# Kernel optimization log

Hardware: AMD Instinct MI355X
Metric: run time of the kernel (lower is better)

Reference implementation:

```python
import jax, jax.numpy as jnp
import numpy as np

B, L, D, NH, DH = 2, 1024, 1024, 16, 2048
HD, HDH = D // NH, DH // NH


def _linear(x, w, b):
    return x @ w.T + b


def _silu(x):
    return x * jax.nn.sigmoid(x)


def _silu_backward(x):
    s = jax.nn.sigmoid(x)
    sil = x * s
    return sil + s * (1.0 - sil)


def setup_inputs() -> dict:
    key = jax.random.key(0)
    ks = jax.random.split(key, 20)
    scale = 0.02
    x = jax.random.normal(ks[0], (B, L, D), dtype=jnp.float32)
    W1 = jax.random.normal(ks[1], (B, NH, HDH, HD), dtype=jnp.float32) * scale
    W2 = jax.random.normal(ks[2], (B, NH, HD, HDH), dtype=jnp.float32) * scale
    log_base_lr = jnp.ones((NH,), jnp.float32) * np.float32(np.log(0.01))
    log_base_weight_decay = jnp.ones((NH,), jnp.float32) * np.float32(np.log(0.1))
    fc_lr_w = jax.random.normal(ks[3], (NH, D), jnp.float32) * scale
    fc_lr_b = jnp.zeros((NH,), jnp.float32)
    fc_wd_w = jax.random.normal(ks[4], (NH, D), jnp.float32) * scale
    fc_wd_b = jnp.zeros((NH,), jnp.float32)
    q_w = jax.random.normal(ks[5], (D, D), jnp.float32) * scale
    q_b = jnp.zeros((D,), jnp.float32)
    k_w = jax.random.normal(ks[6], (D, D), jnp.float32) * scale
    k_b = jnp.zeros((D,), jnp.float32)
    v_w = jax.random.normal(ks[7], (D, D), jnp.float32) * scale
    v_b = jnp.zeros((D,), jnp.float32)
    o_w = jax.random.normal(ks[8], (D, D), jnp.float32) * scale
    o_b = jnp.zeros((D,), jnp.float32)
    return {"x": x, "W1": W1, "W2": W2,
            "log_base_lr": log_base_lr, "fc_lr_w": fc_lr_w, "fc_lr_b": fc_lr_b,
            "log_base_weight_decay": log_base_weight_decay, "fc_wd_w": fc_wd_w, "fc_wd_b": fc_wd_b,
            "q_w": q_w, "q_b": q_b, "k_w": k_w, "k_b": k_b,
            "v_w": v_w, "v_b": v_b, "o_w": o_w, "o_b": o_b}


def reference(x, W1, W2, log_base_lr, fc_lr_w, fc_lr_b, log_base_weight_decay,
              fc_wd_w, fc_wd_b, q_w, q_b, k_w, k_b, v_w, v_b, o_w, o_b):
    batch, length, dim = x.shape
    nh = W1.shape[1]
    hd = dim // nh
    # projections -> [b, n, l, d]
    query = _linear(x, q_w, q_b).reshape(batch, length, nh, hd).transpose(0, 2, 1, 3)
    key = _linear(x, k_w, k_b).reshape(batch, length, nh, hd).transpose(0, 2, 1, 3)
    value = _linear(x, v_w, v_b).reshape(batch, length, nh, hd).transpose(0, 2, 1, 3)
    # per-token, per-head learning rate and weight decay  [b, n, l]
    lr = jnp.exp(log_base_lr)[None, :, None] * jax.nn.sigmoid(_linear(x, fc_lr_w, fc_lr_b)).transpose(0, 2, 1)
    log_wd = jnp.log1p(-jnp.exp(log_base_weight_decay)[None, :, None]
                       * jax.nn.sigmoid(_linear(x, fc_wd_w, fc_wd_b)).transpose(0, 2, 1))
    wd_cross = jnp.exp(jnp.cumsum(log_wd, axis=2))  # [b, n, l]
    # [b, n, m, l] decay mask: exp(sum_{j=m+1}^{l} log_wd_j) on upper triangle
    lw_rep = jnp.broadcast_to(log_wd[:, :, None, :], (batch, nh, length, length))
    wd_inner = jnp.triu(jnp.exp(jnp.cumsum(jnp.triu(lw_rep, 1), axis=3)))
    # two-layer MLP memory forward on keys
    X1 = key
    Z1 = jnp.einsum('bnhd,bnld->bnlh', W1, X1)
    X2 = _silu(Z1)
    Z2 = jnp.einsum('bndh,bnlh->bnld', W2, X2)
    grad_Z2 = Z2 - value
    grad_X2 = jnp.einsum('bndh,bnld->bnlh', W2, grad_Z2)
    grad_Z1 = _silu_backward(Z1) * grad_X2
    # layer-1 readout at queries with chunked delta-rule correction
    X1_ = query
    mask_X1X1_ = jnp.einsum('bnld,bnmd->bnlm', X1, X1_) * wd_inner
    Z1_ = (-jnp.einsum('bnlh,bnl,bnlm->bnmh', grad_Z1, lr, mask_X1X1_)
           + jnp.einsum('bnhd,bnld,bnl->bnlh', W1, X1_, wd_cross))
    W1_next = (-jnp.einsum('bnlh,bnl,bnld->bnhd', grad_Z1, lr * wd_inner[:, :, :, -1], X1)
               + W1 * wd_cross[:, :, -1][:, :, None, None])
    # layer-2 readout
    X2_ = _silu(Z1_)
    mask_X2X2_ = jnp.einsum('bnlh,bnmh->bnlm', X2, X2_) * wd_inner
    Z2_ = (-jnp.einsum('bnld,bnl,bnlm->bnmd', grad_Z2, lr, mask_X2X2_)
           + jnp.einsum('bndh,bnlh,bnl->bnld', W2, X2_, wd_cross))
    W2_next = (-jnp.einsum('bnld,bnl,bnlh->bndh', grad_Z2, lr * wd_inner[:, :, :, -1], X2)
               + W2 * wd_cross[:, :, -1][:, :, None, None])
    out = _linear(Z2_.transpose(0, 2, 1, 3).reshape(batch, length, dim), o_w, o_b)
    return out, W1_next, W2_next
```

## Files before the change

kernel.cpp:

```cpp
#include <hip/hip_runtime.h>

constexpr int CB = 2, CL = 1024, CD = 1024, CNH = 16, CHD = 64, CHDH = 128, CBN = CB * CNH;

__device__ __forceinline__ float sigf(float x) { return 1.0f / (1.0f + __expf(-x)); }

__device__ __forceinline__ unsigned short f2bf(float x) {
    unsigned u = __float_as_uint(x);
    u += 0x7fffu + ((u >> 16) & 1u);
    return (unsigned short)(u >> 16);
}
__device__ __forceinline__ unsigned pk2(float a, float b) {
    return (unsigned)f2bf(a) | ((unsigned)f2bf(b) << 16);
}
__device__ __forceinline__ unsigned pkus(unsigned short a, unsigned short b) {
    return (unsigned)a | ((unsigned)b << 16);
}
__device__ __forceinline__ float bf2f(unsigned short u) {
    return __uint_as_float(((unsigned)u) << 16);
}

typedef __attribute__((ext_vector_type(8))) short short8v;
typedef __attribute__((ext_vector_type(4))) float f32x4;
#define MFMA16(a, b, c) __builtin_amdgcn_mfma_f32_16x16x32_bf16(a, b, c, 0, 0, 0)

__global__ __launch_bounds__(256) void conv_kernel(
    const float* __restrict__ x, const float* __restrict__ qw,
    const float* __restrict__ kw, const float* __restrict__ vw,
    const float* __restrict__ W1, const float* __restrict__ W2,
    const float* __restrict__ ow, unsigned short* __restrict__ xb,
    unsigned short* __restrict__ qwb, unsigned short* __restrict__ kwb,
    unsigned short* __restrict__ vwb, unsigned short* __restrict__ w1b,
    unsigned short* __restrict__ w2b, unsigned short* __restrict__ w2t,
    unsigned short* __restrict__ owh, unsigned short* __restrict__ owl) {
    int i = blockIdx.x * 256 + threadIdx.x;
    if (i < 1310720) {
        const float* s;
        unsigned short* d;
        int off;
        if (i < 524288) { s = x; d = xb; off = i; }
        else if (i < 786432) { s = qw; d = qwb; off = i - 524288; }
        else if (i < 1048576) { s = kw; d = kwb; off = i - 786432; }
        else { s = vw; d = vwb; off = i - 1048576; }
        float4 v = *(const float4*)(s + (size_t)off * 4);
        *(uint2*)(d + (size_t)off * 4) = make_uint2(pk2(v.x, v.y), pk2(v.z, v.w));
    } else if (i < 1507328) {
        int j = i - 1310720;
        if (j < 65536) {
            size_t e = (size_t)j * 4;
            float4 v = *(const float4*)(W1 + e);
            *(uint2*)(w1b + e) = make_uint2(pk2(v.x, v.y), pk2(v.z, v.w));
        } else if (j < 131072) {
            size_t e = (size_t)(j - 65536) * 4;
            float4 v = *(const float4*)(W2 + e);
            *(uint2*)(w2b + e) = make_uint2(pk2(v.x, v.y), pk2(v.z, v.w));
        } else {
            size_t e = (size_t)(j - 131072) * 4;
            int bn = (int)(e >> 13), rem = (int)(e & 8191);
            int h = rem >> 6, d0 = rem & 63;
            const float* src = W2 + (size_t)bn * CHD * CHDH;
            float a = src[(d0 + 0) * CHDH + h], b = src[(d0 + 1) * CHDH + h];
            float c = src[(d0 + 2) * CHDH + h], dd = src[(d0 + 3) * CHDH + h];
            *(uint2*)(w2t + e) = make_uint2(pk2(a, b), pk2(c, dd));
        }
    } else {
        size_t e = (size_t)(i - 1507328) * 4;
        float4 v = *(const float4*)(ow + e);
        unsigned short h0 = f2bf(v.x), h1 = f2bf(v.y), h2 = f2bf(v.z), h3 = f2bf(v.w);
        *(uint2*)(owh + e) = make_uint2(pkus(h0, h1), pkus(h2, h3));
        *(uint2*)(owl + e) = make_uint2(
            pk2(v.x - bf2f(h0), v.y - bf2f(h1)), pk2(v.z - bf2f(h2), v.w - bf2f(h3)));
    }
}

__global__ __launch_bounds__(512) void qkv_mfma(
    const unsigned short* __restrict__ xbf, const unsigned short* __restrict__ wqkv,
    const float* __restrict__ qb, const float* __restrict__ kb,
    const float* __restrict__ vb, unsigned short* __restrict__ qbf,
    unsigned short* __restrict__ kbf, unsigned short* __restrict__ ktbf,
    float* __restrict__ vhb) {
    __shared__ __align__(16) unsigned short SM[26112];
    unsigned short(*Ab)[136] = (unsigned short(*)[136])SM;
    unsigned short(*Bb)[136] = (unsigned short(*)[136])(SM + 8704);
    const int t = threadIdx.x;
    const int c0 = blockIdx.x << 7, r0 = blockIdx.y << 6;
    const int wv = t >> 6, lane = t & 63;
    const int lm = lane & 15, lg = lane >> 4;
    f32x4 acc[4];
#pragma unroll
    for (int i = 0; i < 4; ++i) acc[i] = (f32x4){0.f, 0.f, 0.f, 0.f};
    for (int kc = 0; kc < CD; kc += 128) {
        for (int i = t; i < 1024; i += 512) {
            int r = i >> 4, c = (i & 15) * 8;
            *(uint4*)&Ab[r][c] = *(const uint4*)(xbf + (size_t)(r0 + r) * CD + kc + c);
        }
        for (int i = t; i < 2048; i += 512) {
            int r = i >> 4, c = (i & 15) * 8;
            *(uint4*)&Bb[r][c] = *(const uint4*)(wqkv + (size_t)(c0 + r) * CD + kc + c);
        }
        __syncthreads();
#pragma unroll
        for (int m16 = 0; m16 < 4; ++m16)
#pragma unroll
            for (int ks = 0; ks < 4; ++ks) {
                short8v a = *(const short8v*)&Ab[m16 * 16 + lm][ks * 32 + lg * 8];
                short8v b = *(const short8v*)&Bb[wv * 16 + lm][ks * 32 + lg * 8];
                acc[m16] = MFMA16(a, b, acc[m16]);
            }
        __syncthreads();
    }
    const int which = c0 >> 10;
    const int ccb = c0 & 1023;
    const float* bias = which == 0 ? qb : (which == 1 ? kb : vb);
    const int b = r0 >> 10, lb0 = r0 & 1023;
    float(*Os)[132] = (float(*)[132])SM;
    {
        int col = wv * 16 + lm;
        float bb = bias[ccb + col];
#pragma unroll
        for (int m16 = 0; m16 < 4; ++m16)
#pragma unroll
            for (int r = 0; r < 4; ++r)
                Os[m16 * 16 + lg * 4 + r][col] = acc[m16][r] + bb;
    }
    __syncthreads();
    if (which == 2) {
        for (int i = t; i < 2048; i += 512) {
            int r = i >> 5, c = (i & 31) * 4;
            int n = (ccb + c) >> 6, d = (ccb + c) & 63;
            *(float4*)(vhb + (((size_t)b * CNH + n) * CL + lb0 + r) * 64 + d) =
                *(const float4*)&Os[r][c];
        }
    } else {
        unsigned short* dst = which == 0 ? qbf : kbf;
        for (int i = t; i < 2048; i += 512) {
            int r = i >> 5, c = (i & 31) * 4;
            int n = (ccb + c) >> 6, d = (ccb + c) & 63;
            float4 v4 = *(const float4*)&Os[r][c];
            *(uint2*)(dst + (((size_t)b * CNH + n) * CL + lb0 + r) * 64 + d) =
                make_uint2(pk2(v4.x, v4.y), pk2(v4.z, v4.w));
        }
        if (which == 1) {
            for (int i = t; i < 1024; i += 512) {
                int col = i >> 3, lb = (i & 7) * 8;
                int n = (ccb + col) >> 6, d = (ccb + col) & 63;
                uint4 u;
                u.x = pk2(Os[lb + 0][col], Os[lb + 1][col]);
                u.y = pk2(Os[lb + 2][col], Os[lb + 3][col]);
                u.z = pk2(Os[lb + 4][col], Os[lb + 5][col]);
                u.w = pk2(Os[lb + 6][col], Os[lb + 7][col]);
                *(uint4*)(ktbf + (((size_t)b * CNH + n) * 64 + d) * CL + lb0 + lb) = u;
            }
        }
    }
}

__global__ __launch_bounds__(512) void gemm_obf(const unsigned short* __restrict__ zh,
                                                const unsigned short* __restrict__ zl,
                                                const unsigned short* __restrict__ Bh,
                                                const unsigned short* __restrict__ Bl,
                                                const float* __restrict__ bias,
                                                float* __restrict__ C) {
    __shared__ __align__(16) unsigned short SM[52224];
    unsigned short(*Ah)[136] = (unsigned short(*)[136])SM;
    unsigned short(*Al)[136] = (unsigned short(*)[136])(SM + 8704);
    unsigned short(*Bhs)[136] = (unsigned short(*)[136])(SM + 17408);
    unsigned short(*Bls)[136] = (unsigned short(*)[136])(SM + 34816);
    const int t = threadIdx.x;
    const int r0 = blockIdx.x << 6, c0 = blockIdx.y << 7;
    const int wv = t >> 6, lane = t & 63;
    const int lm = lane & 15, lg = lane >> 4;
    const int b = r0 >> 10, lb0 = r0 & 1023;
    f32x4 acc[4];
#pragma unroll
    for (int i = 0; i < 4; ++i) acc[i] = (f32x4){0.f, 0.f, 0.f, 0.f};
    for (int kc = 0; kc < CD; kc += 128) {
        for (int i = t; i < 1024; i += 512) {
            int r = i >> 4, c = (i & 15) * 8;
            int k = kc + c, n = k >> 6, d = k & 63;
            size_t abase = (((size_t)b * CNH + n) * CL + lb0 + r) * 64 + d;
            *(uint4*)&Ah[r][c] = *(const uint4*)(zh + abase);
            *(uint4*)&Al[r][c] = *(const uint4*)(zl + abase);
        }
        for (int i = t; i < 2048; i += 512) {
            int r = i >> 4, c = (i & 15) * 8;
            *(uint4*)&Bhs[r][c] = *(const uint4*)(Bh + (size_t)(c0 + r) * CD + kc + c);
            *(uint4*)&Bls[r][c] = *(const uint4*)(Bl + (size_t)(c0 + r) * CD + kc + c);
        }
        __syncthreads();
#pragma unroll
        for (int m16 = 0; m16 < 4; ++m16)
#pragma unroll
            for (int ks = 0; ks < 4; ++ks) {
                short8v ah = *(const short8v*)&Ah[m16 * 16 + lm][ks * 32 + lg * 8];
                short8v al = *(const short8v*)&Al[m16 * 16 + lm][ks * 32 + lg * 8];
                short8v bh = *(const short8v*)&Bhs[wv * 16 + lm][ks * 32 + lg * 8];
                short8v bl = *(const short8v*)&Bls[wv * 16 + lm][ks * 32 + lg * 8];
                acc[m16] = MFMA16(ah, bh, acc[m16]);
                acc[m16] = MFMA16(ah, bl, acc[m16]);
                acc[m16] = MFMA16(al, bh, acc[m16]);
            }
        __syncthreads();
    }
    float(*Os)[132] = (float(*)[132])SM;
    {
        int col = wv * 16 + lm;
        float bb = bias[c0 + col];
#pragma unroll
        for (int m16 = 0; m16 < 4; ++m16)
#pragma unroll
            for (int r = 0; r < 4; ++r)
                Os[m16 * 16 + lg * 4 + r][col] = acc[m16][r] + bb;
    }
    __syncthreads();
    for (int i = t; i < 2048; i += 512) {
        int r = i >> 5, c = (i & 31) * 4;
        *(float4*)(C + (size_t)(r0 + r) * CD + c0 + c) = *(const float4*)&Os[r][c];
    }
}

__global__ __launch_bounds__(256) void lrwd_kernel(
    const float* __restrict__ x, const float* __restrict__ lblr,
    const float* __restrict__ fclr_w, const float* __restrict__ fclr_b,
    const float* __restrict__ lbwd, const float* __restrict__ fcwd_w,
    const float* __restrict__ fcwd_b, float* __restrict__ lrp,
    float* __restrict__ logwd) {
    const int r = blockIdx.x;
    const int b = r >> 10, l = r & 1023;
    const int wv = threadIdx.x >> 6, lane = threadIdx.x & 63;
    float xv[16];
#pragma unroll
    for (int j = 0; j < 16; ++j) xv[j] = x[(size_t)r * CD + lane + 64 * j];
    for (int j = 0; j < 4; ++j) {
        const int n = wv * 4 + j;
        float d1 = 0.f, d2 = 0.f;
#pragma unroll
        for (int k = 0; k < 16; ++k) {
            d1 += xv[k] * fclr_w[(size_t)n * CD + lane + 64 * k];
            d2 += xv[k] * fcwd_w[(size_t)n * CD + lane + 64 * k];
        }
#pragma unroll
        for (int s = 32; s > 0; s >>= 1) {
            d1 += __shfl_down(d1, s);
            d2 += __shfl_down(d2, s);
        }
        if (lane == 0) {
            lrp[((size_t)b * CNH + n) * CL + l] = __expf(lblr[n]) * sigf(d1 + fclr_b[n]);
            logwd[((size_t)b * CNH + n) * CL + l] =
                log1pf(-__expf(lbwd[n]) * sigf(d2 + fcwd_b[n]));
        }
    }
}

__global__ __launch_bounds__(64) void scan_kernel(float* __restrict__ cum,
                                                  float* __restrict__ wdc) {
    const int bn = blockIdx.x;
    const int lane = threadIdx.x;
    float* p = cum + (size_t)bn * CL;
    float v[16];
#pragma unroll
    for (int j = 0; j < 16; ++j) v[j] = p[lane * 16 + j];
#pragma unroll
    for (int j = 1; j < 16; ++j) v[j] += v[j - 1];
    float tot = v[15];
    float inc = tot;
#pragma unroll
    for (int s = 1; s < 64; s <<= 1) {
        float tv = __shfl_up(inc, s);
        if (lane >= s) inc += tv;
    }
    const float pre = inc - tot;
#pragma unroll
    for (int j = 0; j < 16; ++j) {
        float c = pre + v[j];
        p[lane * 16 + j] = c;
        wdc[(size_t)bn * CL + lane * 16 + j] = __expf(c);
    }
}

__global__ __launch_bounds__(256) void mlp_mfma(
    const unsigned short* __restrict__ kbf, const float* __restrict__ vh,
    const unsigned short* __restrict__ w1bf, const unsigned short* __restrict__ w2bf,
    const unsigned short* __restrict__ w2tbf, unsigned short* __restrict__ x2bf,
    unsigned short* __restrict__ x2t, unsigned short* __restrict__ gz1t,
    unsigned short* __restrict__ gz2t) {
    __shared__ __align__(16) unsigned short RA[128][72];
    __shared__ __align__(16) unsigned short RB[64][72];
    __shared__ __align__(16) unsigned short RC[64][136];
    __shared__ __align__(16) unsigned short X2s[64][136];
    const int bn = blockIdx.y, l0 = blockIdx.x << 6;
    const int t = threadIdx.x;
    const int wv = t >> 6, lane = t & 63;
    const int lm = lane & 15, lg = lane >> 4;
    {
        const unsigned short* kg = kbf + ((size_t)bn * CL + l0) * CHD;
        for (int i = t; i < 512; i += 256) {
            int r = i >> 3, c = (i & 7) * 8;
            *(uint4*)&RB[r][c] = *(const uint4*)(kg + (size_t)r * CHD + c);
        }
        const unsigned short* w1g = w1bf + (size_t)bn * CHDH * CHD;
        for (int i = t; i < 1024; i += 256) {
            int r = i >> 3, c = (i & 7) * 8;
            *(uint4*)&RA[r][c] = *(const uint4*)(w1g + (size_t)r * CHD + c);
        }
        const unsigned short* w2g = w2bf + (size_t)bn * CHD * CHDH;
        for (int i = t; i < 1024; i += 256) {
            int r = i >> 4, c = (i & 15) * 8;
            *(uint4*)&RC[r][c] = *(const uint4*)(w2g + (size_t)r * CHDH + c);
        }
    }
    __syncthreads();
    f32x4 acc1[4][2];
#pragma unroll
    for (int i = 0; i < 4; ++i)
#pragma unroll
        for (int j = 0; j < 2; ++j) acc1[i][j] = (f32x4){0.f, 0.f, 0.f, 0.f};
#pragma unroll
    for (int m16 = 0; m16 < 4; ++m16)
#pragma unroll
        for (int hh = 0; hh < 2; ++hh) {
            int h16 = wv * 2 + hh;
#pragma unroll
            for (int ks = 0; ks < 2; ++ks) {
                short8v a = *(const short8v*)&RB[m16 * 16 + lm][ks * 32 + lg * 8];
                short8v b = *(const short8v*)&RA[h16 * 16 + lm][ks * 32 + lg * 8];
                acc1[m16][hh] = MFMA16(a, b, acc1[m16][hh]);
            }
        }
#pragma unroll
    for (int m16 = 0; m16 < 4; ++m16)
#pragma unroll
        for (int hh = 0; hh < 2; ++hh)
#pragma unroll
            for (int r = 0; r < 4; ++r) {
                float a = acc1[m16][hh][r];
                X2s[m16 * 16 + lg * 4 + r][(wv * 2 + hh) * 16 + lm] = f2bf(a * sigf(a));
            }
    __syncthreads();
    {
        const unsigned short* w2tg = w2tbf + (size_t)bn * CHDH * CHD;
        for (int i = t; i < 1024; i += 256) {
            int r = i >> 3, c = (i & 7) * 8;
            *(uint4*)&RA[r][c] = *(const uint4*)(w2tg + (size_t)r * CHD + c);
        }
    }
    {
        f32x4 acc2[4];
#pragma unroll
        for (int i = 0; i < 4; ++i) acc2[i] = (f32x4){0.f, 0.f, 0.f, 0.f};
#pragma unroll
        for (int m16 = 0; m16 < 4; ++m16)
#pragma unroll
            for (int ks = 0; ks < 4; ++ks) {
                short8v a = *(const short8v*)&X2s[m16 * 16 + lm][ks * 32 + lg * 8];
                short8v b = *(const short8v*)&RC[wv * 16 + lm][ks * 32 + lg * 8];
                acc2[m16] = MFMA16(a, b, acc2[m16]);
            }
#pragma unroll
        for (int m16 = 0; m16 < 4; ++m16)
#pragma unroll
            for (int r = 0; r < 4; ++r) {
                int l = l0 + m16 * 16 + lg * 4 + r;
                float v = vh[((size_t)bn * CL + l) * 64 + wv * 16 + lm];
                RB[m16 * 16 + lg * 4 + r][wv * 16 + lm] = f2bf(acc2[m16][r] - v);
            }
    }
    __syncthreads();
#pragma unroll
    for (int m16 = 0; m16 < 4; ++m16)
#pragma unroll
        for (int hh = 0; hh < 2; ++hh) {
            int h16 = wv * 2 + hh;
            f32x4 p = (f32x4){0.f, 0.f, 0.f, 0.f};
#pragma unroll
            for (int ks = 0; ks < 2; ++ks) {
                short8v a = *(const short8v*)&RB[m16 * 16 + lm][ks * 32 + lg * 8];
                short8v b = *(const short8v*)&RA[h16 * 16 + lm][ks * 32 + lg * 8];
                p = MFMA16(a, b, p);
            }
#pragma unroll
            for (int r = 0; r < 4; ++r) {
                float zz = acc1[m16][hh][r];
                float s = sigf(zz);
                float sil = zz * s;
                RC[m16 * 16 + lg * 4 + r][h16 * 16 + lm] =
                    f2bf((sil + s * (1.f - sil)) * p[r]);
            }
        }
    __syncthreads();
    for (int i = t; i < 1024; i += 256) {
        int r = i >> 4, c = (i & 15) * 8;
        *(uint4*)(x2bf + ((size_t)bn * CL + l0 + r) * CHDH + c) = *(const uint4*)&X2s[r][c];
    }
    for (int i = t; i < 1024; i += 256) {
        int h = i >> 3, lb = (i & 7) * 8;
        uint4 u;
        u.x = pkus(X2s[lb + 0][h], X2s[lb + 1][h]);
        u.y = pkus(X2s[lb + 2][h], X2s[lb + 3][h]);
        u.z = pkus(X2s[lb + 4][h], X2s[lb + 5][h]);
        u.w = pkus(X2s[lb + 6][h], X2s[lb + 7][h]);
        *(uint4*)(x2t + ((size_t)bn * CHDH + h) * CL + l0 + lb) = u;
    }
    for (int i = t; i < 1024; i += 256) {
        int h = i >> 3, lb = (i & 7) * 8;
        uint4 u;
        u.x = pkus(RC[lb + 0][h], RC[lb + 1][h]);
        u.y = pkus(RC[lb + 2][h], RC[lb + 3][h]);
        u.z = pkus(RC[lb + 4][h], RC[lb + 5][h]);
        u.w = pkus(RC[lb + 6][h], RC[lb + 7][h]);
        *(uint4*)(gz1t + ((size_t)bn * CHDH + h) * CL + l0 + lb) = u;
    }
    for (int i = t; i < 512; i += 256) {
        int d = i >> 3, lb = (i & 7) * 8;
        uint4 u;
        u.x = pkus(RB[lb + 0][d], RB[lb + 1][d]);
        u.y = pkus(RB[lb + 2][d], RB[lb + 3][d]);
        u.z = pkus(RB[lb + 4][d], RB[lb + 5][d]);
        u.w = pkus(RB[lb + 6][d], RB[lb + 7][d]);
        *(uint4*)(gz2t + ((size_t)bn * CHD + d) * CL + l0 + lb) = u;
    }
}

__global__ __launch_bounds__(256) void dsA1(
    const unsigned short* __restrict__ ktbf, const unsigned short* __restrict__ gz1t,
    const float* __restrict__ lrp, const float* __restrict__ cump,
    float* __restrict__ ds1, float* __restrict__ ds2) {
    __shared__ __align__(16) unsigned short Ab[64][72];
    __shared__ __align__(16) unsigned short Bb[128][72];
    __shared__ float coefA[64];
    const int c = blockIdx.x, bn = blockIdx.y, t = threadIdx.x;
    const int l0 = c << 6;
    const int wv = t >> 6, lane = t & 63;
    const int lm = lane & 15, lg = lane >> 4;
    const float Ac = cump[(size_t)bn * CL + l0];
    if (t < 64)
        coefA[t] = lrp[(size_t)bn * CL + l0 + t] *
                   __expf(Ac - cump[(size_t)bn * CL + l0 + t]);
    for (int i = t; i < 1024; i += 256) {
        int h = i >> 3, cc = (i & 7) * 8;
        *(uint4*)&Bb[h][cc] = *(const uint4*)(gz1t + ((size_t)bn * CHDH + h) * CL + l0 + cc);
    }
    __syncthreads();
    for (int i = t; i < 512; i += 256) {
        int d = i >> 3, cc = (i & 7) * 8;
        uint4 g = *(const uint4*)(ktbf + ((size_t)bn * CHD + d) * CL + l0 + cc);
        unsigned short* gp = (unsigned short*)&g;
        uint4 o;
        o.x = pk2(bf2f(gp[0]) * coefA[cc + 0], bf2f(gp[1]) * coefA[cc + 1]);
        o.y = pk2(bf2f(gp[2]) * coefA[cc + 2], bf2f(gp[3]) * coefA[cc + 3]);
        o.z = pk2(bf2f(gp[4]) * coefA[cc + 4], bf2f(gp[5]) * coefA[cc + 5]);
        o.w = pk2(bf2f(gp[6]) * coefA[cc + 6], bf2f(gp[7]) * coefA[cc + 7]);
        *(uint4*)&Ab[d][cc] = o;
    }
    __syncthreads();
    f32x4 acc[8];
#pragma unroll
    for (int i = 0; i < 8; ++i) acc[i] = (f32x4){0.f, 0.f, 0.f, 0.f};
#pragma unroll
    for (int h16 = 0; h16 < 8; ++h16)
#pragma unroll
        for (int ks = 0; ks < 2; ++ks) {
            short8v a = *(const short8v*)&Ab[wv * 16 + lm][ks * 32 + lg * 8];
            short8v b = *(const short8v*)&Bb[h16 * 16 + lm][ks * 32 + lg * 8];
            acc[h16] = MFMA16(a, b, acc[h16]);
        }
    float* og = (bn < 16 ? ds1 : ds2) + ((size_t)(((bn & 15) << 4) + c) << 13);
#pragma unroll
    for (int h16 = 0; h16 < 8; ++h16)
#pragma unroll
        for (int r = 0; r < 4; ++r)
            og[(wv * 16 + lg * 4 + r) * 128 + h16 * 16 + lm] = acc[h16][r];
}

__global__ __launch_bounds__(256) void dsB1(
    const float* __restrict__ ds1, const float* __restrict__ ds2,
    const float* __restrict__ cump, const float* __restrict__ W1,
    unsigned short* __restrict__ sp1, float* __restrict__ w1n) {
    __shared__ float anch[16];
    const int g = blockIdx.x, bn = blockIdx.y, t = threadIdx.x;
    if (t < 16) anch[t] = cump[(size_t)bn * CL + (t << 6)];
    __syncthreads();
    const float ccl = cump[(size_t)bn * CL + CL - 1];
    const float wdcl = __expf(ccl);
    const float* dS = (bn < 16 ? ds1 : ds2) + ((size_t)((bn & 15) << 4) << 13);
    unsigned short* spb = sp1 + ((size_t)bn << 17);
    const int e0 = g << 10;
    float s[4];
#pragma unroll
    for (int j = 0; j < 4; ++j) s[j] = 0.f;
    for (int c = 0; c < 16; ++c) {
        if (c > 0) {
            float fac = __expf(anch[c] - anch[c - 1]);
            const float* dp = dS + ((size_t)(c - 1) << 13);
#pragma unroll
            for (int j = 0; j < 4; ++j) s[j] = fac * (s[j] + dp[e0 + j * 256 + t]);
        }
        unsigned short* so = spb + ((size_t)c << 13);
#pragma unroll
        for (int j = 0; j < 4; ++j) so[e0 + j * 256 + t] = f2bf(s[j]);
    }
    const float ex = __expf(ccl - anch[15]);
    const float* dp = dS + ((size_t)15 << 13);
    const float* w1g = W1 + ((size_t)bn << 13);
    float* og = w1n + ((size_t)bn << 13);
#pragma unroll
    for (int j = 0; j < 4; ++j) {
        int e = e0 + j * 256 + t;
        int d = e >> 7, h = e & 127;
        float full = s[j] + dp[e];
        og[h * 64 + d] = wdcl * w1g[h * 64 + d] - ex * full;
    }
}

__global__ __launch_bounds__(256) void dsC1(
    const unsigned short* __restrict__ qbf, const unsigned short* __restrict__ kbf,
    const unsigned short* __restrict__ gz1t, const unsigned short* __restrict__ w1bf,
    const unsigned short* __restrict__ sp1, const float* __restrict__ lrp,
    const float* __restrict__ cump, const float* __restrict__ wdcp,
    unsigned short* __restrict__ x2q) {
    __shared__ __align__(16) unsigned short Qb[64][72];
    __shared__ __align__(16) unsigned short XB[128][72];
    __shared__ __align__(16) unsigned short Kb[64][72];
    __shared__ __align__(16) unsigned short GT[128][72];
    __shared__ __align__(16) unsigned short Pm[64][72];
    __shared__ float lrc[64], cumc[64], wdcc[64];
    const int c = blockIdx.x, bn = blockIdx.y, t = threadIdx.x;
    const int l0 = c << 6;
    const int w4 = t >> 6, lane = t & 63;
    const int lm = lane & 15, lg = lane >> 4;
    {
        const unsigned short* qg = qbf + ((size_t)bn * CL + l0) * CHD;
        for (int i = t; i < 512; i += 256) {
            int r = i >> 3, cc = (i & 7) * 8;
            *(uint4*)&Qb[r][cc] = *(const uint4*)(qg + (size_t)r * CHD + cc);
        }
        const unsigned short* wg = w1bf + (size_t)bn * CHDH * CHD;
        for (int i = t; i < 1024; i += 256) {
            int r = i >> 3, cc = (i & 7) * 8;
            *(uint4*)&XB[r][cc] = *(const uint4*)(wg + (size_t)r * CHD + cc);
        }
        if (t < 64) {
            lrc[t] = lrp[(size_t)bn * CL + l0 + t];
            cumc[t] = cump[(size_t)bn * CL + l0 + t];
            wdcc[t] = wdcp[(size_t)bn * CL + l0 + t];
        }
    }
    __syncthreads();
    const float Ac = cumc[0];
    short8v qf[4][2];
#pragma unroll
    for (int m16 = 0; m16 < 4; ++m16)
#pragma unroll
        for (int ks = 0; ks < 2; ++ks)
            qf[m16][ks] = *(const short8v*)&Qb[m16 * 16 + lm][ks * 32 + lg * 8];
    f32x4 acc[4][2];
#pragma unroll
    for (int i = 0; i < 4; ++i)
#pragma unroll
        for (int j = 0; j < 2; ++j) acc[i][j] = (f32x4){0.f, 0.f, 0.f, 0.f};
    {
        short8v wf[2][2];
#pragma unroll
        for (int hh = 0; hh < 2; ++hh)
#pragma unroll
            for (int ks = 0; ks < 2; ++ks)
                wf[hh][ks] =
                    *(const short8v*)&XB[(w4 * 2 + hh) * 16 + lm][ks * 32 + lg * 8];
#pragma unroll
        for (int m16 = 0; m16 < 4; ++m16)
#pragma unroll
            for (int hh = 0; hh < 2; ++hh)
#pragma unroll
                for (int ks = 0; ks < 2; ++ks)
                    acc[m16][hh] = MFMA16(qf[m16][ks], wf[hh][ks], acc[m16][hh]);
#pragma unroll
        for (int m16 = 0; m16 < 4; ++m16)
#pragma unroll
            for (int r = 0; r < 4; ++r) {
                float w = wdcc[m16 * 16 + lg * 4 + r];
                acc[m16][0][r] *= w;
                acc[m16][1][r] *= w;
            }
    }
    __syncthreads();
    {
        const unsigned short* sb = sp1 + ((((size_t)bn << 4) + c) << 13);
        for (int i = t; i < 1024; i += 256) {
            int d = i >> 4, hg = (i & 15) * 8;
            uint4 u = *(const uint4*)(sb + d * 128 + hg);
            const unsigned short* up = (const unsigned short*)&u;
#pragma unroll
            for (int j = 0; j < 8; ++j) XB[hg + j][d] = up[j];
        }
    }
    __syncthreads();
    {
        short8v sf[2][2];
#pragma unroll
        for (int hh = 0; hh < 2; ++hh)
#pragma unroll
            for (int ks = 0; ks < 2; ++ks)
                sf[hh][ks] =
                    *(const short8v*)&XB[(w4 * 2 + hh) * 16 + lm][ks * 32 + lg * 8];
#pragma unroll
        for (int m16 = 0; m16 < 4; ++m16)
#pragma unroll
            for (int hh = 0; hh < 2; ++hh) {
                f32x4 pf = (f32x4){0.f, 0.f, 0.f, 0.f};
#pragma unroll
                for (int ks = 0; ks < 2; ++ks)
                    pf = MFMA16(qf[m16][ks], sf[hh][ks], pf);
#pragma unroll
                for (int r = 0; r < 4; ++r) {
                    float em = __expf(cumc[m16 * 16 + lg * 4 + r] - Ac);
                    acc[m16][hh][r] -= em * pf[r];
                }
            }
    }
    __syncthreads();
    {
        const unsigned short* kg = kbf + ((size_t)bn * CL + l0) * CHD;
        for (int i = t; i < 512; i += 256) {
            int r = i >> 3, cc = (i & 7) * 8;
            *(uint4*)&Kb[r][cc] = *(const uint4*)(kg + (size_t)r * CHD + cc);
        }
        const unsigned short* gg = gz1t + (size_t)bn * CHDH * CL + l0;
        for (int i = t; i < 1024; i += 256) {
            int r = i >> 3, cc = (i & 7) * 8;
            *(uint4*)&GT[r][cc] = *(const uint4*)(gg + (size_t)r * CL + cc);
        }
    }
    __syncthreads();
    {
        short8v kf[2];
#pragma unroll
        for (int ks = 0; ks < 2; ++ks)
            kf[ks] = *(const short8v*)&Kb[w4 * 16 + lm][ks * 32 + lg * 8];
#pragma unroll
        for (int m16 = 0; m16 < 4; ++m16) {
            f32x4 s = (f32x4){0.f, 0.f, 0.f, 0.f};
#pragma unroll
            for (int ks = 0; ks < 2; ++ks) s = MFMA16(kf[ks], qf[m16][ks], s);
            int mloc = m16 * 16 + lm;
            float cm = cumc[mloc];
            unsigned short pv[4];
#pragma unroll
            for (int r = 0; r < 4; ++r) {
                int lloc = w4 * 16 + lg * 4 + r;
                float val = (mloc >= lloc)
                                ? s[r] * lrc[lloc] * __expf(cm - cumc[lloc])
                                : 0.f;
                pv[r] = f2bf(val);
            }
            *(uint2*)&Pm[mloc][w4 * 16 + lg * 4] =
                make_uint2(pkus(pv[0], pv[1]), pkus(pv[2], pv[3]));
        }
    }
    __syncthreads();
    {
        short8v gt[2][2], pm[4][2];
#pragma unroll
        for (int hh = 0; hh < 2; ++hh)
#pragma unroll
            for (int ks = 0; ks < 2; ++ks)
                gt[hh][ks] =
                    *(const short8v*)&GT[(w4 * 2 + hh) * 16 + lm][ks * 32 + lg * 8];
#pragma unroll
        for (int m16 = 0; m16 < 4; ++m16)
#pragma unroll
            for (int ks = 0; ks < 2; ++ks)
                pm[m16][ks] = *(const short8v*)&Pm[m16 * 16 + lm][ks * 32 + lg * 8];
#pragma unroll
        for (int m16 = 0; m16 < 4; ++m16)
#pragma unroll
            for (int hh = 0; hh < 2; ++hh) {
                f32x4 pf = (f32x4){0.f, 0.f, 0.f, 0.f};
#pragma unroll
                for (int ks = 0; ks < 2; ++ks) pf = MFMA16(pm[m16][ks], gt[hh][ks], pf);
#pragma unroll
                for (int r = 0; r < 4; ++r) acc[m16][hh][r] -= pf[r];
            }
    }
    __syncthreads();
    {
        unsigned short(*Ob)[136] = (unsigned short(*)[136])XB;
#pragma unroll
        for (int m16 = 0; m16 < 4; ++m16)
#pragma unroll
            for (int hh = 0; hh < 2; ++hh) {
                int h = (w4 * 2 + hh) * 16 + lm;
#pragma unroll
                for (int r = 0; r < 4; ++r) {
                    float a = acc[m16][hh][r];
                    Ob[m16 * 16 + lg * 4 + r][h] = f2bf(a * sigf(a));
                }
            }
        __syncthreads();
        unsigned short* og = x2q + ((size_t)bn * CL + l0) * CHDH;
        for (int i = t; i < 1024; i += 256) {
            int r = i >> 4, cc = (i & 15) * 8;
            *(uint4*)(og + (size_t)r * CHDH + cc) = *(const uint4*)&Ob[r][cc];
        }
    }
}

__global__ __launch_bounds__(256) void dsA2(
    const unsigned short* __restrict__ x2t, const unsigned short* __restrict__ gz2t,
    const float* __restrict__ lrp, const float* __restrict__ cump,
    float* __restrict__ ds1, float* __restrict__ ds2) {
    __shared__ __align__(16) unsigned short Ab[128][72];
    __shared__ __align__(16) unsigned short Bb[64][72];
    __shared__ float coefA[64];
    const int c = blockIdx.x, bn = blockIdx.y, t = threadIdx.x;
    const int l0 = c << 6;
    const int wv = t >> 6, lane = t & 63;
    const int lm = lane & 15, lg = lane >> 4;
    const float Ac = cump[(size_t)bn * CL + l0];
    if (t < 64)
        coefA[t] = lrp[(size_t)bn * CL + l0 + t] *
                   __expf(Ac - cump[(size_t)bn * CL + l0 + t]);
    for (int i = t; i < 512; i += 256) {
        int d = i >> 3, cc = (i & 7) * 8;
        *(uint4*)&Bb[d][cc] = *(const uint4*)(gz2t + ((size_t)bn * CHD + d) * CL + l0 + cc);
    }
    __syncthreads();
    for (int i = t; i < 1024; i += 256) {
        int h = i >> 3, cc = (i & 7) * 8;
        uint4 g = *(const uint4*)(x2t + ((size_t)bn * CHDH + h) * CL + l0 + cc);
        unsigned short* gp = (unsigned short*)&g;
        uint4 o;
        o.x = pk2(bf2f(gp[0]) * coefA[cc + 0], bf2f(gp[1]) * coefA[cc + 1]);
        o.y = pk2(bf2f(gp[2]) * coefA[cc + 2], bf2f(gp[3]) * coefA[cc + 3]);
        o.z = pk2(bf2f(gp[4]) * coefA[cc + 4], bf2f(gp[5]) * coefA[cc + 5]);
        o.w = pk2(bf2f(gp[6]) * coefA[cc + 6], bf2f(gp[7]) * coefA[cc + 7]);
        *(uint4*)&Ab[h][cc] = o;
    }
    __syncthreads();
    f32x4 acc[2][4];
#pragma unroll
    for (int i = 0; i < 2; ++i)
#pragma unroll
        for (int j = 0; j < 4; ++j) acc[i][j] = (f32x4){0.f, 0.f, 0.f, 0.f};
#pragma unroll
    for (int mm = 0; mm < 2; ++mm) {
        int hk16 = wv * 2 + mm;
#pragma unroll
        for (int d16 = 0; d16 < 4; ++d16)
#pragma unroll
            for (int ks = 0; ks < 2; ++ks) {
                short8v a = *(const short8v*)&Ab[hk16 * 16 + lm][ks * 32 + lg * 8];
                short8v b = *(const short8v*)&Bb[d16 * 16 + lm][ks * 32 + lg * 8];
                acc[mm][d16] = MFMA16(a, b, acc[mm][d16]);
            }
    }
    float* og = (bn < 16 ? ds1 : ds2) + ((size_t)(((bn & 15) << 4) + c) << 13);
#pragma unroll
    for (int mm = 0; mm < 2; ++mm)
#pragma unroll
        for (int d16 = 0; d16 < 4; ++d16)
#pragma unroll
            for (int r = 0; r < 4; ++r)
                og[((wv * 2 + mm) * 16 + lg * 4 + r) * 64 + d16 * 16 + lm] =
                    acc[mm][d16][r];
}

__global__ __launch_bounds__(256) void dsB2(
    const float* __restrict__ ds1, const float* __restrict__ ds2,
    const float* __restrict__ cump, const float* __restrict__ W2,
    unsigned short* __restrict__ sp2, float* __restrict__ w2n) {
    __shared__ float anch[16];
    const int g = blockIdx.x, bn = blockIdx.y, t = threadIdx.x;
    if (t < 16) anch[t] = cump[(size_t)bn * CL + (t << 6)];
    __syncthreads();
    const float ccl = cump[(size_t)bn * CL + CL - 1];
    const float wdcl = __expf(ccl);
    const float* dS = (bn < 16 ? ds1 : ds2) + ((size_t)((bn & 15) << 4) << 13);
    unsigned short* spb = sp2 + ((size_t)bn << 17);
    const int e0 = g << 10;
    float s[4];
#pragma unroll
    for (int j = 0; j < 4; ++j) s[j] = 0.f;
    for (int c = 0; c < 16; ++c) {
        if (c > 0) {
            float fac = __expf(anch[c] - anch[c - 1]);
            const float* dp = dS + ((size_t)(c - 1) << 13);
#pragma unroll
            for (int j = 0; j < 4; ++j) s[j] = fac * (s[j] + dp[e0 + j * 256 + t]);
        }
        unsigned short* so = spb + ((size_t)c << 13);
#pragma unroll
        for (int j = 0; j < 4; ++j) so[e0 + j * 256 + t] = f2bf(s[j]);
    }
    const float ex = __expf(ccl - anch[15]);
    const float* dp = dS + ((size_t)15 << 13);
    const float* w2g = W2 + ((size_t)bn << 13);
    float* og = w2n + ((size_t)bn << 13);
#pragma unroll
    for (int j = 0; j < 4; ++j) {
        int e = e0 + j * 256 + t;
        int hk = e >> 6, d = e & 63;
        float full = s[j] + dp[e];
        og[d * 128 + hk] = wdcl * w2g[d * 128 + hk] - ex * full;
    }
}

__global__ __launch_bounds__(256) void dsC2(
    const unsigned short* __restrict__ x2q, const unsigned short* __restrict__ x2bf,
    const unsigned short* __restrict__ gz2t, const unsigned short* __restrict__ w2bf,
    const unsigned short* __restrict__ sp2, const float* __restrict__ lrp,
    const float* __restrict__ cump, const float* __restrict__ wdcp,
    unsigned short* __restrict__ zh, unsigned short* __restrict__ zl) {
    __shared__ __align__(16) unsigned short X2qb[64][136];
    __shared__ __align__(16) unsigned short XB[64][136];
    __shared__ __align__(16) unsigned short GT2[64][72];
    __shared__ __align__(16) unsigned short Pm[64][72];
    __shared__ float lrc[64], cumc[64], wdcc[64];
    const int c = blockIdx.x, bn = blockIdx.y, t = threadIdx.x;
    const int l0 = c << 6;
    const int w4 = t >> 6, lane = t & 63;
    const int lm = lane & 15, lg = lane >> 4;
    {
        const unsigned short* qg = x2q + ((size_t)bn * CL + l0) * CHDH;
        for (int i = t; i < 1024; i += 256) {
            int r = i >> 4, cc = (i & 15) * 8;
            *(uint4*)&X2qb[r][cc] = *(const uint4*)(qg + (size_t)r * CHDH + cc);
        }
        const unsigned short* wg = w2bf + (size_t)bn * CHD * CHDH;
        for (int i = t; i < 1024; i += 256) {
            int r = i >> 4, cc = (i & 15) * 8;
            *(uint4*)&XB[r][cc] = *(const uint4*)(wg + (size_t)r * CHDH + cc);
        }
        if (t < 64) {
            lrc[t] = lrp[(size_t)bn * CL + l0 + t];
            cumc[t] = cump[(size_t)bn * CL + l0 + t];
            wdcc[t] = wdcp[(size_t)bn * CL + l0 + t];
        }
    }
    __syncthreads();
    const float Ac = cumc[0];
    short8v qf[4][4];
#pragma unroll
    for (int m16 = 0; m16 < 4; ++m16)
#pragma unroll
        for (int ks = 0; ks < 4; ++ks)
            qf[m16][ks] = *(const short8v*)&X2qb[m16 * 16 + lm][ks * 32 + lg * 8];
    f32x4 acc[4];
#pragma unroll
    for (int i = 0; i < 4; ++i) acc[i] = (f32x4){0.f, 0.f, 0.f, 0.f};
    {
        short8v wf[4];
#pragma unroll
        for (int ks = 0; ks < 4; ++ks)
            wf[ks] = *(const short8v*)&XB[w4 * 16 + lm][ks * 32 + lg * 8];
#pragma unroll
        for (int m16 = 0; m16 < 4; ++m16)
#pragma unroll
            for (int ks = 0; ks < 4; ++ks)
                acc[m16] = MFMA16(qf[m16][ks], wf[ks], acc[m16]);
#pragma unroll
        for (int m16 = 0; m16 < 4; ++m16)
#pragma unroll
            for (int r = 0; r < 4; ++r)
                acc[m16][r] *= wdcc[m16 * 16 + lg * 4 + r];
    }
    __syncthreads();
    {
        const unsigned short* sb = sp2 + ((((size_t)bn << 4) + c) << 13);
        for (int i = t; i < 1024; i += 256) {
            int hk = i >> 3, dg = (i & 7) * 8;
            uint4 u = *(const uint4*)(sb + hk * 64 + dg);
            const unsigned short* up = (const unsigned short*)&u;
#pragma unroll
            for (int j = 0; j < 8; ++j) XB[dg + j][hk] = up[j];
        }
    }
    __syncthreads();
    {
        short8v sf[4];
#pragma unroll
        for (int ks = 0; ks < 4; ++ks)
            sf[ks] = *(const short8v*)&XB[w4 * 16 + lm][ks * 32 + lg * 8];
#pragma unroll
        for (int m16 = 0; m16 < 4; ++m16) {
            f32x4 pf = (f32x4){0.f, 0.f, 0.f, 0.f};
#pragma unroll
            for (int ks = 0; ks < 4; ++ks) pf = MFMA16(qf[m16][ks], sf[ks], pf);
#pragma unroll
            for (int r = 0; r < 4; ++r) {
                float em = __expf(cumc[m16 * 16 + lg * 4 + r] - Ac);
                acc[m16][r] -= em * pf[r];
            }
        }
    }
    __syncthreads();
    {
        const unsigned short* kg = x2bf + ((size_t)bn * CL + l0) * CHDH;
        for (int i = t; i < 1024; i += 256) {
            int r = i >> 4, cc = (i & 15) * 8;
            *(uint4*)&XB[r][cc] = *(const uint4*)(kg + (size_t)r * CHDH + cc);
        }
        const unsigned short* gg = gz2t + (size_t)bn * CHD * CL + l0;
        for (int i = t; i < 512; i += 256) {
            int r = i >> 3, cc = (i & 7) * 8;
            *(uint4*)&GT2[r][cc] = *(const uint4*)(gg + (size_t)r * CL + cc);
        }
    }
    __syncthreads();
    {
        short8v kf[4];
#pragma unroll
        for (int ks = 0; ks < 4; ++ks)
            kf[ks] = *(const short8v*)&XB[w4 * 16 + lm][ks * 32 + lg * 8];
#pragma unroll
        for (int m16 = 0; m16 < 4; ++m16) {
            f32x4 s = (f32x4){0.f, 0.f, 0.f, 0.f};
#pragma unroll
            for (int ks = 0; ks < 4; ++ks) s = MFMA16(kf[ks], qf[m16][ks], s);
            int mloc = m16 * 16 + lm;
            float cm = cumc[mloc];
            unsigned short pv[4];
#pragma unroll
            for (int r = 0; r < 4; ++r) {
                int lloc = w4 * 16 + lg * 4 + r;
                float val = (mloc >= lloc)
                                ? s[r] * lrc[lloc] * __expf(cm - cumc[lloc])
                                : 0.f;
                pv[r] = f2bf(val);
            }
            *(uint2*)&Pm[mloc][w4 * 16 + lg * 4] =
                make_uint2(pkus(pv[0], pv[1]), pkus(pv[2], pv[3]));
        }
    }
    __syncthreads();
    {
        short8v gt[2], pm[4][2];
#pragma unroll
        for (int ks = 0; ks < 2; ++ks)
            gt[ks] = *(const short8v*)&GT2[w4 * 16 + lm][ks * 32 + lg * 8];
#pragma unroll
        for (int m16 = 0; m16 < 4; ++m16)
#pragma unroll
            for (int ks = 0; ks < 2; ++ks)
                pm[m16][ks] = *(const short8v*)&Pm[m16 * 16 + lm][ks * 32 + lg * 8];
#pragma unroll
        for (int m16 = 0; m16 < 4; ++m16) {
            f32x4 pf = (f32x4){0.f, 0.f, 0.f, 0.f};
#pragma unroll
            for (int ks = 0; ks < 2; ++ks) pf = MFMA16(pm[m16][ks], gt[ks], pf);
#pragma unroll
            for (int r = 0; r < 4; ++r) acc[m16][r] -= pf[r];
        }
    }
    __syncthreads();
    {
        float(*Os)[68] = (float(*)[68])X2qb;
#pragma unroll
        for (int m16 = 0; m16 < 4; ++m16)
#pragma unroll
            for (int r = 0; r < 4; ++r)
                Os[m16 * 16 + lg * 4 + r][w4 * 16 + lm] = acc[m16][r];
        __syncthreads();
        unsigned short* zhg = zh + ((size_t)bn * CL + l0) * CHD;
        unsigned short* zlg = zl + ((size_t)bn * CL + l0) * CHD;
        for (int i = t; i < 1024; i += 256) {
            int r = i >> 4, cc = (i & 15) << 2;
            float4 v = *(const float4*)&Os[r][cc];
            unsigned short h0 = f2bf(v.x), h1 = f2bf(v.y), h2 = f2bf(v.z), h3 = f2bf(v.w);
            *(uint2*)(zhg + (size_t)r * CHD + cc) = make_uint2(pkus(h0, h1), pkus(h2, h3));
            *(uint2*)(zlg + (size_t)r * CHD + cc) = make_uint2(
                pk2(v.x - bf2f(h0), v.y - bf2f(h1)), pk2(v.z - bf2f(h2), v.w - bf2f(h3)));
        }
    }
}

extern "C" void kernel_launch(void* const* d_in, const int* in_sizes, int n_in,
                              void* d_out, int out_size, void* d_ws, size_t ws_size,
                              hipStream_t stream) {
    (void)in_sizes; (void)n_in; (void)out_size; (void)ws_size;
    const float* x      = (const float*)d_in[0];
    const float* W1     = (const float*)d_in[1];
    const float* W2     = (const float*)d_in[2];
    const float* lblr   = (const float*)d_in[3];
    const float* fclr_w = (const float*)d_in[4];
    const float* fclr_b = (const float*)d_in[5];
    const float* lbwd   = (const float*)d_in[6];
    const float* fcwd_w = (const float*)d_in[7];
    const float* fcwd_b = (const float*)d_in[8];
    const float* qw = (const float*)d_in[9];
    const float* qb = (const float*)d_in[10];
    const float* kw = (const float*)d_in[11];
    const float* kb = (const float*)d_in[12];
    const float* vw = (const float*)d_in[13];
    const float* vb = (const float*)d_in[14];
    const float* ow = (const float*)d_in[15];
    const float* ob = (const float*)d_in[16];

    float* ws = (float*)d_ws;
    const size_t SZ_HD = (size_t)CBN * CL * CHD;
    const size_t SZ_HDH = (size_t)CBN * CL * CHDH;
    float* qh   = ws;
    float* khb  = qh + SZ_HD;
    float* vhb  = khb + SZ_HD;
    float* gz2b = vhb + SZ_HD;
    float* z2sb = gz2b + SZ_HD;
    float* x2b  = z2sb + SZ_HD;
    float* gz1b = x2b + SZ_HDH;
    float* x2qb = gz1b + SZ_HDH;
    float* lrb  = x2qb + SZ_HDH;
    float* cumb = lrb + (size_t)CBN * CL;
    float* wdcb = cumb + (size_t)CBN * CL;
    unsigned short* xbf  = (unsigned short*)(wdcb + (size_t)CBN * CL);
    unsigned short* qwbf = xbf + (size_t)CB * CL * CD;
    unsigned short* kwbf = qwbf + (size_t)CD * CD;
    unsigned short* vwbf = kwbf + (size_t)CD * CD;
    unsigned short* owh  = vwbf + (size_t)CD * CD;
    unsigned short* owl  = owh + (size_t)CD * CD;

    unsigned short* qbf   = (unsigned short*)qh;
    unsigned short* kbf   = qbf + SZ_HD;
    unsigned short* ktbf  = (unsigned short*)khb;
    unsigned short* w1bf  = ktbf + SZ_HD;
    unsigned short* w2bf  = w1bf + (size_t)CBN * CHDH * CHD;
    unsigned short* w2tbf = w2bf + (size_t)CBN * CHDH * CHD;
    unsigned short* gz2t  = (unsigned short*)gz2b;
    unsigned short* x2t   = (unsigned short*)x2b;
    unsigned short* gz1t  = (unsigned short*)gz1b;
    unsigned short* x2q   = (unsigned short*)x2qb;
    unsigned short* x2bf  = x2q + SZ_HDH;
    float* ds1 = gz1b + 2097152;
    float* ds2 = x2b + 2097152;
    unsigned short* sp1 = (unsigned short*)vhb;
    unsigned short* sp2 = (unsigned short*)vhb;
    unsigned short* zh = (unsigned short*)z2sb;
    unsigned short* zl = zh + SZ_HD;

    float* outp = (float*)d_out;
    float* w1n = outp + (size_t)CB * CL * CD;
    float* w2n = w1n + (size_t)CBN * CHDH * CHD;

    conv_kernel<<<6912, 256, 0, stream>>>(x, qw, kw, vw, W1, W2, ow, xbf, qwbf, kwbf,
                                          vwbf, w1bf, w2bf, w2tbf, owh, owl);
    qkv_mfma<<<dim3(24, 32), 512, 0, stream>>>(xbf, qwbf, qb, kb, vb, qbf, kbf, ktbf,
                                               vhb);
    lrwd_kernel<<<CB * CL, 256, 0, stream>>>(x, lblr, fclr_w, fclr_b, lbwd, fcwd_w,
                                             fcwd_b, lrb, cumb);
    scan_kernel<<<CBN, 64, 0, stream>>>(cumb, wdcb);
    mlp_mfma<<<dim3(CL / 64, CBN), 256, 0, stream>>>(kbf, vhb, w1bf, w2bf, w2tbf,
                                                     x2bf, x2t, gz1t, gz2t);
    dsA1<<<dim3(16, CBN), 256, 0, stream>>>(ktbf, gz1t, lrb, cumb, ds1, ds2);
    dsB1<<<dim3(8, CBN), 256, 0, stream>>>(ds1, ds2, cumb, W1, sp1, w1n);
    dsC1<<<dim3(16, CBN), 256, 0, stream>>>(qbf, kbf, gz1t, w1bf, sp1, lrb, cumb,
                                            wdcb, x2q);
    dsA2<<<dim3(16, CBN), 256, 0, stream>>>(x2t, gz2t, lrb, cumb, ds1, ds2);
    dsB2<<<dim3(8, CBN), 256, 0, stream>>>(ds1, ds2, cumb, W2, sp2, w2n);
    dsC2<<<dim3(16, CBN), 256, 0, stream>>>(x2q, x2bf, gz2t, w2bf, sp2, lrb, cumb,
                                            wdcb, zh, zl);
    gemm_obf<<<dim3(32, 8), 512, 0, stream>>>(zh, zl, owh, owl, ob, outp);
}
```

Measured before the change: 168.6 us.

## Prefetch all chunk operands into dedicated LDS buffers and drop intermediate barriers

In the two chunked readout kernels (dsC1 and dsC2), the single reused LDS staging buffer is split into separate buffers for W, the chunk state, keys and the transposed gradient. All of these are loaded at kernel start instead of in staged phases, which removes several __syncthreads barriers and lets the global loads overlap with each other. The cost is much more LDS per block, which can cut how many blocks fit on a CU. The removal of some barriers before aliased output staging also depends on later barriers for correctness.

Result: slower. 180.6 us (+7.1%).

```diff
diff --git a/kernel.cpp b/kernel.cpp
--- a/kernel.cpp
+++ b/kernel.cpp
@@ -518,7 +518,8 @@
     const float* __restrict__ cump, const float* __restrict__ wdcp,
     unsigned short* __restrict__ x2q) {
     __shared__ __align__(16) unsigned short Qb[64][72];
-    __shared__ __align__(16) unsigned short XB[128][72];
+    __shared__ __align__(16) unsigned short W1b[128][72];
+    __shared__ __align__(16) unsigned short S1[128][72];
     __shared__ __align__(16) unsigned short Kb[64][72];
     __shared__ __align__(16) unsigned short GT[128][72];
     __shared__ __align__(16) unsigned short Pm[64][72];
@@ -536,7 +537,25 @@
         const unsigned short* wg = w1bf + (size_t)bn * CHDH * CHD;
         for (int i = t; i < 1024; i += 256) {
             int r = i >> 3, cc = (i & 7) * 8;
-            *(uint4*)&XB[r][cc] = *(const uint4*)(wg + (size_t)r * CHD + cc);
+            *(uint4*)&W1b[r][cc] = *(const uint4*)(wg + (size_t)r * CHD + cc);
+        }
+        const unsigned short* sb = sp1 + ((((size_t)bn << 4) + c) << 13);
+        for (int i = t; i < 1024; i += 256) {
+            int d = i >> 4, hg = (i & 15) * 8;
+            uint4 u = *(const uint4*)(sb + d * 128 + hg);
+            const unsigned short* up = (const unsigned short*)&u;
+#pragma unroll
+            for (int j = 0; j < 8; ++j) S1[hg + j][d] = up[j];
+        }
+        const unsigned short* kg = kbf + ((size_t)bn * CL + l0) * CHD;
+        for (int i = t; i < 512; i += 256) {
+            int r = i >> 3, cc = (i & 7) * 8;
+            *(uint4*)&Kb[r][cc] = *(const uint4*)(kg + (size_t)r * CHD + cc);
+        }
+        const unsigned short* gg = gz1t + (size_t)bn * CHDH * CL + l0;
+        for (int i = t; i < 1024; i += 256) {
+            int r = i >> 3, cc = (i & 7) * 8;
+            *(uint4*)&GT[r][cc] = *(const uint4*)(gg + (size_t)r * CL + cc);
         }
         if (t < 64) {
             lrc[t] = lrp[(size_t)bn * CL + l0 + t];
@@ -564,7 +583,7 @@
 #pragma unroll
             for (int ks = 0; ks < 2; ++ks)
                 wf[hh][ks] =
-                    *(const short8v*)&XB[(w4 * 2 + hh) * 16 + lm][ks * 32 + lg * 8];
+                    *(const short8v*)&W1b[(w4 * 2 + hh) * 16 + lm][ks * 32 + lg * 8];
 #pragma unroll
         for (int m16 = 0; m16 < 4; ++m16)
 #pragma unroll
@@ -581,18 +600,6 @@
                 acc[m16][1][r] *= w;
             }
     }
-    __syncthreads();
-    {
-        const unsigned short* sb = sp1 + ((((size_t)bn << 4) + c) << 13);
-        for (int i = t; i < 1024; i += 256) {
-            int d = i >> 4, hg = (i & 15) * 8;
-            uint4 u = *(const uint4*)(sb + d * 128 + hg);
-            const unsigned short* up = (const unsigned short*)&u;
-#pragma unroll
-            for (int j = 0; j < 8; ++j) XB[hg + j][d] = up[j];
-        }
-    }
-    __syncthreads();
     {
         short8v sf[2][2];
 #pragma unroll
@@ -600,7 +607,7 @@
 #pragma unroll
             for (int ks = 0; ks < 2; ++ks)
                 sf[hh][ks] =
-                    *(const short8v*)&XB[(w4 * 2 + hh) * 16 + lm][ks * 32 + lg * 8];
+                    *(const short8v*)&S1[(w4 * 2 + hh) * 16 + lm][ks * 32 + lg * 8];
 #pragma unroll
         for (int m16 = 0; m16 < 4; ++m16)
 #pragma unroll
@@ -616,20 +623,6 @@
                 }
             }
     }
-    __syncthreads();
-    {
-        const unsigned short* kg = kbf + ((size_t)bn * CL + l0) * CHD;
-        for (int i = t; i < 512; i += 256) {
-            int r = i >> 3, cc = (i & 7) * 8;
-            *(uint4*)&Kb[r][cc] = *(const uint4*)(kg + (size_t)r * CHD + cc);
-        }
-        const unsigned short* gg = gz1t + (size_t)bn * CHDH * CL + l0;
-        for (int i = t; i < 1024; i += 256) {
-            int r = i >> 3, cc = (i & 7) * 8;
-            *(uint4*)&GT[r][cc] = *(const uint4*)(gg + (size_t)r * CL + cc);
-        }
-    }
-    __syncthreads();
     {
         short8v kf[2];
 #pragma unroll
@@ -680,9 +673,8 @@
                 for (int r = 0; r < 4; ++r) acc[m16][hh][r] -= pf[r];
             }
     }
-    __syncthreads();
-    {
-        unsigned short(*Ob)[136] = (unsigned short(*)[136])XB;
+    {
+        unsigned short(*Ob)[136] = (unsigned short(*)[136])S1;
 #pragma unroll
         for (int m16 = 0; m16 < 4; ++m16)
 #pragma unroll
@@ -810,7 +802,9 @@
     const float* __restrict__ cump, const float* __restrict__ wdcp,
     unsigned short* __restrict__ zh, unsigned short* __restrict__ zl) {
     __shared__ __align__(16) unsigned short X2qb[64][136];
-    __shared__ __align__(16) unsigned short XB[64][136];
+    __shared__ __align__(16) unsigned short W2b[64][136];
+    __shared__ __align__(16) unsigned short S2[64][136];
+    __shared__ __align__(16) unsigned short Kx[64][136];
     __shared__ __align__(16) unsigned short GT2[64][72];
     __shared__ __align__(16) unsigned short Pm[64][72];
     __shared__ float lrc[64], cumc[64], wdcc[64];
@@ -827,7 +821,25 @@
         const unsigned short* wg = w2bf + (size_t)bn * CHD * CHDH;
         for (int i = t; i < 1024; i += 256) {
             int r = i >> 4, cc = (i & 15) * 8;
-            *(uint4*)&XB[r][cc] = *(const uint4*)(wg + (size_t)r * CHDH + cc);
+            *(uint4*)&W2b[r][cc] = *(const uint4*)(wg + (size_t)r * CHDH + cc);
+        }
+        const unsigned short* sb = sp2 + ((((size_t)bn << 4) + c) << 13);
+        for (int i = t; i < 1024; i += 256) {
+            int hk = i >> 3, dg = (i & 7) * 8;
+            uint4 u = *(const uint4*)(sb + hk * 64 + dg);
+            const unsigned short* up = (const unsigned short*)&u;
+#pragma unroll
+            for (int j = 0; j < 8; ++j) S2[dg + j][hk] = up[j];
+        }
+        const unsigned short* kg = x2bf + ((size_t)bn * CL + l0) * CHDH;
+        for (int i = t; i < 1024; i += 256) {
+            int r = i >> 4, cc = (i & 15) * 8;
+            *(uint4*)&Kx[r][cc] = *(const uint4*)(kg + (size_t)r * CHDH + cc);
+        }
+        const unsigned short* gg = gz2t + (size_t)bn * CHD * CL + l0;
+        for (int i = t; i < 512; i += 256) {
+            int r = i >> 3, cc = (i & 7) * 8;
+            *(uint4*)&GT2[r][cc] = *(const uint4*)(gg + (size_t)r * CL + cc);
         }
         if (t < 64) {
             lrc[t] = lrp[(size_t)bn * CL + l0 + t];
@@ -850,7 +862,7 @@
         short8v wf[4];
 #pragma unroll
         for (int ks = 0; ks < 4; ++ks)
-            wf[ks] = *(const short8v*)&XB[w4 * 16 + lm][ks * 32 + lg * 8];
+            wf[ks] = *(const short8v*)&W2b[w4 * 16 + lm][ks * 32 + lg * 8];
 #pragma unroll
         for (int m16 = 0; m16 < 4; ++m16)
 #pragma unroll
@@ -862,23 +874,11 @@
             for (int r = 0; r < 4; ++r)
                 acc[m16][r] *= wdcc[m16 * 16 + lg * 4 + r];
     }
-    __syncthreads();
-    {
-        const unsigned short* sb = sp2 + ((((size_t)bn << 4) + c) << 13);
-        for (int i = t; i < 1024; i += 256) {
-            int hk = i >> 3, dg = (i & 7) * 8;
-            uint4 u = *(const uint4*)(sb + hk * 64 + dg);
-            const unsigned short* up = (const unsigned short*)&u;
-#pragma unroll
-            for (int j = 0; j < 8; ++j) XB[dg + j][hk] = up[j];
-        }
-    }
-    __syncthreads();
     {
         short8v sf[4];
 #pragma unroll
         for (int ks = 0; ks < 4; ++ks)
-            sf[ks] = *(const short8v*)&XB[w4 * 16 + lm][ks * 32 + lg * 8];
+            sf[ks] = *(const short8v*)&S2[w4 * 16 + lm][ks * 32 + lg * 8];
 #pragma unroll
         for (int m16 = 0; m16 < 4; ++m16) {
             f32x4 pf = (f32x4){0.f, 0.f, 0.f, 0.f};
@@ -891,25 +891,11 @@
             }
         }
     }
-    __syncthreads();
-    {
-        const unsigned short* kg = x2bf + ((size_t)bn * CL + l0) * CHDH;
-        for (int i = t; i < 1024; i += 256) {
-            int r = i >> 4, cc = (i & 15) * 8;
-            *(uint4*)&XB[r][cc] = *(const uint4*)(kg + (size_t)r * CHDH + cc);
-        }
-        const unsigned short* gg = gz2t + (size_t)bn * CHD * CL + l0;
-        for (int i = t; i < 512; i += 256) {
-            int r = i >> 3, cc = (i & 7) * 8;
-            *(uint4*)&GT2[r][cc] = *(const uint4*)(gg + (size_t)r * CL + cc);
-        }
-    }
-    __syncthreads();
     {
         short8v kf[4];
 #pragma unroll
         for (int ks = 0; ks < 4; ++ks)
-            kf[ks] = *(const short8v*)&XB[w4 * 16 + lm][ks * 32 + lg * 8];
+            kf[ks] = *(const short8v*)&Kx[w4 * 16 + lm][ks * 32 + lg * 8];
 #pragma unroll
         for (int m16 = 0; m16 < 4; ++m16) {
             f32x4 s = (f32x4){0.f, 0.f, 0.f, 0.f};
@@ -950,7 +936,6 @@
             for (int r = 0; r < 4; ++r) acc[m16][r] -= pf[r];
         }
     }
-    __syncthreads();
     {
         float(*Os)[68] = (float(*)[68])X2qb;
 #pragma unroll
```
